# Optimization experiments

Hardware: AMD Instinct MI355X
Metric: run time of the kernel (lower is better)

## Reference

```python
import jax, jax.numpy as jnp
import numpy as np

B, F, H, E, O = 512, 512, 512, 8, 512  # batch, feature, hidden, experts, out_frame


def setup_inputs() -> dict:
    key = jax.random.key(0)
    ks = jax.random.split(key, 14)
    u = lambda k, shape, s: jax.random.uniform(k, shape, jnp.float32) * s
    return {
        "x": jax.random.normal(ks[0], (B, F), jnp.float32),
        # gating MLP params (torch Linear: y = x @ W.T + b)
        "gw0": u(ks[1], (H, F), 0.04) - 0.02,
        "gb0": jnp.zeros((H,), jnp.float32),
        "gw1": u(ks[2], (H, H), 0.04) - 0.02,
        "gb1": jnp.zeros((H,), jnp.float32),
        "gw2": u(ks[3], (E, H), 0.04) - 0.02,
        "gb2": jnp.zeros((E,), jnp.float32),
        # expert weight/bias banks
        "alpha0": u(ks[4], (E, H, F), 0.01),
        "beta0": jnp.zeros((E, H, 1), jnp.float32),
        "alpha1": u(ks[5], (E, H, H), 0.01),
        "beta1": jnp.zeros((E, H, 1), jnp.float32),
        "alpha2": u(ks[6], (E, O, H), 0.01),
        "beta2": jnp.zeros((E, O, 1), jnp.float32),
    }


def reference(x, gw0, gb0, gw1, gb1, gw2, gb2,
              alpha0, beta0, alpha1, beta1, alpha2, beta2):
    # gating network
    h = jax.nn.elu(x @ gw0.T + gb0)
    h = jax.nn.elu(h @ gw1.T + gb1)
    g = jax.nn.softmax(h @ gw2.T + gb2, axis=1)  # [B, E]

    # per-sample blended weights (sum over experts of gate-scaled expert mats)
    blend_w = lambda a: jnp.einsum('be,ehf->bhf', g, a)
    blend_b = lambda b: jnp.einsum('be,eh->bh', g, b[..., 0])

    # per-sample 3-layer MLP (bmm with vector rhs == batched matvec)
    H1 = jax.nn.elu(jnp.einsum('bhf,bf->bh', blend_w(alpha0), x) + blend_b(beta0))
    H2 = jax.nn.elu(jnp.einsum('bhf,bf->bh', blend_w(alpha1), H1) + blend_b(beta1))
    H3 = jnp.einsum('bof,bf->bo', blend_w(alpha2), H2) + blend_b(beta2)
    return H3
```

## Files before the change

### kernel.cpp

```cpp
#include <hip/hip_runtime.h>
#include <hip/hip_bf16.h>
#include <math.h>

enum { Bq = 512, Fq = 512, Hq = 512, Eq = 8, Oq = 512 };

typedef __attribute__((ext_vector_type(8))) short short8;
typedef __attribute__((ext_vector_type(4))) float floatx4;

static __device__ __forceinline__ unsigned short f2bf(float f) {
  unsigned u = __float_as_uint(f);
  u += 0x7fffu + ((u >> 16) & 1u);
  return (unsigned short)(u >> 16);
}
static __device__ __forceinline__ float bf2f(unsigned short h) {
  return __uint_as_float(((unsigned)h) << 16);
}
static __device__ __forceinline__ float elu1(float v) {
  return v > 0.f ? v : (__expf(v) - 1.f);
}

typedef __attribute__((address_space(1))) const unsigned int gu32;
typedef __attribute__((address_space(3))) unsigned int lu32;
static __device__ __forceinline__ void gld16(const unsigned short* g,
                                             unsigned short* l) {
  __builtin_amdgcn_global_load_lds((gu32*)g, (lu32*)l, 16, 0, 0);
}

__global__ __launch_bounds__(256) void cvt6_kernel(
    const float* __restrict__ b0, const float* __restrict__ b1,
    const float* __restrict__ b2, unsigned short* __restrict__ db0,
    unsigned short* __restrict__ db1, unsigned short* __restrict__ db2,
    const float* __restrict__ s0, const float* __restrict__ s1,
    const float* __restrict__ s2, unsigned short* __restrict__ ds0,
    unsigned short* __restrict__ ds1, unsigned short* __restrict__ ds2,
    int nb, int ns) {
  int i = blockIdx.x * 256 + threadIdx.x;
  const float4* s;
  unsigned short* d;
  int j;
  if (i < 3 * nb) {
    int seg = i / nb;
    j = i - seg * nb;
    s = (seg == 0) ? (const float4*)b0
      : (seg == 1) ? (const float4*)b1 : (const float4*)b2;
    d = (seg == 0) ? db0 : (seg == 1) ? db1 : db2;
  } else {
    int k = i - 3 * nb;
    if (k >= 3 * ns) return;
    int seg = k / ns;
    j = k - seg * ns;
    s = (seg == 0) ? (const float4*)s0
      : (seg == 1) ? (const float4*)s1 : (const float4*)s2;
    d = (seg == 0) ? ds0 : (seg == 1) ? ds1 : ds2;
  }
  float4 v = s[j];
  ushort4 o;
  o.x = f2bf(v.x); o.y = f2bf(v.y); o.z = f2bf(v.z); o.w = f2bf(v.w);
  *(ushort4*)(d + 4 * (size_t)j) = o;
}

template <int BM, int BN, int BK, int TM, int TN>
__global__ __launch_bounds__(256) void gemm_bt(
    const unsigned short* __restrict__ A, const unsigned short* __restrict__ W,
    const float* __restrict__ bias, unsigned short* __restrict__ Cb,
    int M, int N, int K) {
  __shared__ unsigned short As[BM * BK];
  __shared__ unsigned short Bs[BN * BK];
  const int tid = threadIdx.x;
  const int wave = tid >> 6, lane = tid & 63;
  const int wm = wave >> 1, wn = wave & 1;
  const int lr = lane & 15, lk = lane >> 4;
  const int m0 = blockIdx.y * BM, n0 = blockIdx.x * BN;
  constexpr int WMt = BM / 2, WNt = BN / 2;
  constexpr int CPR = BK / 8;
  constexpr int CHA = BM * CPR, CHB = BN * CPR;

  floatx4 acc[TM][TN];
#pragma unroll
  for (int i = 0; i < TM; i++)
#pragma unroll
    for (int j = 0; j < TN; j++) acc[i][j] = (floatx4){0.f, 0.f, 0.f, 0.f};

  for (int k0 = 0; k0 < K; k0 += BK) {
#pragma unroll
    for (int c = tid; c < CHA; c += 256) {
      int r = c / CPR, q = c % CPR;
      gld16(&A[(size_t)(m0 + r) * K + k0 + q * 8], &As[(c & ~63) * 8]);
    }
#pragma unroll
    for (int c = tid; c < CHB; c += 256) {
      int r = c / CPR, q = c % CPR;
      gld16(&W[(size_t)(n0 + r) * K + k0 + q * 8], &Bs[(c & ~63) * 8]);
    }
    __syncthreads();
#pragma unroll
    for (int kk = 0; kk < BK; kk += 32) {
      short8 af[TM], bw[TN];
#pragma unroll
      for (int i = 0; i < TM; i++)
        af[i] = *(const short8*)&As[(wm * WMt + i * 16 + lr) * BK + kk + lk * 8];
#pragma unroll
      for (int j = 0; j < TN; j++)
        bw[j] = *(const short8*)&Bs[(wn * WNt + j * 16 + lr) * BK + kk + lk * 8];
#pragma unroll
      for (int i = 0; i < TM; i++)
#pragma unroll
        for (int j = 0; j < TN; j++)
          acc[i][j] = __builtin_amdgcn_mfma_f32_16x16x32_bf16(
              af[i], bw[j], acc[i][j], 0, 0, 0);
    }
    __syncthreads();
  }

#pragma unroll
  for (int i = 0; i < TM; i++) {
#pragma unroll
    for (int j = 0; j < TN; j++) {
#pragma unroll
      for (int r = 0; r < 4; r++) {
        int m = m0 + wm * WMt + i * 16 + lk * 4 + r;
        int n = n0 + wn * WNt + j * 16 + lr;
        float v = acc[i][j][r] + bias[n];
        Cb[(size_t)m * N + n] = f2bf(elu1(v));
      }
    }
  }
}

template <int BM, int BN, int BK, int TM, int TN>
__global__ __launch_bounds__(256) void expert_gemm(
    const unsigned short* __restrict__ A,
    const unsigned short* __restrict__ Wb,
    const float* __restrict__ g,
    float* __restrict__ P) {
  __shared__ unsigned short As[BM * BK];
  __shared__ unsigned short Bs[BN * BK];
  const int tid = threadIdx.x;
  const int wave = tid >> 6, lane = tid & 63;
  const int wm = wave >> 1, wn = wave & 1;
  const int lr = lane & 15, lk = lane >> 4;
  const int m0 = blockIdx.y * BM, n0 = blockIdx.x * BN;
  const int e = blockIdx.z >> 1, ks = blockIdx.z & 1;
  const int kbeg = ks * 256, kend = kbeg + 256;
  const unsigned short* W = Wb + (size_t)e * Hq * 512 + (size_t)n0 * 512;
  constexpr int WMt = BM / 2, WNt = BN / 2;
  constexpr int CPR = BK / 8;
  constexpr int CHA = BM * CPR, CHB = BN * CPR;

  floatx4 acc[TM][TN];
#pragma unroll
  for (int i = 0; i < TM; i++)
#pragma unroll
    for (int j = 0; j < TN; j++) acc[i][j] = (floatx4){0.f, 0.f, 0.f, 0.f};

  for (int k0 = kbeg; k0 < kend; k0 += BK) {
#pragma unroll
    for (int c = tid; c < CHA; c += 256) {
      int r = c / CPR, q = c % CPR;
      gld16(&A[(size_t)(m0 + r) * 512 + k0 + q * 8], &As[(c & ~63) * 8]);
    }
#pragma unroll
    for (int c = tid; c < CHB; c += 256) {
      int r = c / CPR, q = c % CPR;
      gld16(&W[(size_t)r * 512 + k0 + q * 8], &Bs[(c & ~63) * 8]);
    }
    __syncthreads();
#pragma unroll
    for (int kk = 0; kk < BK; kk += 32) {
      short8 af[TM], bw[TN];
#pragma unroll
      for (int i = 0; i < TM; i++)
        af[i] = *(const short8*)&As[(wm * WMt + i * 16 + lr) * BK + kk + lk * 8];
#pragma unroll
      for (int j = 0; j < TN; j++)
        bw[j] = *(const short8*)&Bs[(wn * WNt + j * 16 + lr) * BK + kk + lk * 8];
#pragma unroll
      for (int i = 0; i < TM; i++)
#pragma unroll
        for (int j = 0; j < TN; j++)
          acc[i][j] = __builtin_amdgcn_mfma_f32_16x16x32_bf16(
              af[i], bw[j], acc[i][j], 0, 0, 0);
    }
    __syncthreads();
  }

  float* Po = P + (size_t)blockIdx.z * Bq * Hq;
#pragma unroll
  for (int i = 0; i < TM; i++) {
#pragma unroll
    for (int j = 0; j < TN; j++) {
#pragma unroll
      for (int r = 0; r < 4; r++) {
        int m = m0 + wm * WMt + i * 16 + lk * 4 + r;
        int n = n0 + wn * WNt + j * 16 + lr;
        Po[(size_t)m * Hq + n] = acc[i][j][r] * g[m * Eq + e];
      }
    }
  }
}

__global__ __launch_bounds__(64) void gate_kernel(
    const unsigned short* __restrict__ G1,
    const float* __restrict__ gw2,
    const float* __restrict__ gb2,
    float* __restrict__ g) {
  int b = blockIdx.x;
  int lane = threadIdx.x;
  float xv[8];
#pragma unroll
  for (int t = 0; t < 8; t++) xv[t] = bf2f(G1[(size_t)b * Hq + t * 64 + lane]);
  float le[Eq];
#pragma unroll
  for (int e = 0; e < Eq; e++) {
    float p = 0.f;
#pragma unroll
    for (int t = 0; t < 8; t++)
      p += xv[t] * gw2[(size_t)e * Hq + t * 64 + lane];
#pragma unroll
    for (int o = 32; o > 0; o >>= 1) p += __shfl_xor(p, o);
    le[e] = p + gb2[e];
  }
  float m = le[0];
#pragma unroll
  for (int e = 1; e < Eq; e++) m = fmaxf(m, le[e]);
  float s = 0.f;
#pragma unroll
  for (int e = 0; e < Eq; e++) {
    le[e] = __expf(le[e] - m);
    s += le[e];
  }
  float inv = 1.f / s;
  if (lane == 0) {
#pragma unroll
    for (int e = 0; e < Eq; e++) g[(size_t)b * Eq + e] = le[e] * inv;
  }
}

template <int ACT>
__global__ __launch_bounds__(256) void reduce_kernel(
    const float* __restrict__ P,
    const float* __restrict__ g,
    const float* __restrict__ beta,
    unsigned short* __restrict__ outb, float* __restrict__ outf) {
  int idx = blockIdx.x * 256 + threadIdx.x;
  int b = idx >> 7, h4 = (idx & 127) << 2;
  float4 s = {0.f, 0.f, 0.f, 0.f};
#pragma unroll
  for (int z = 0; z < 16; z++) {
    float4 v = *(const float4*)&P[((size_t)z * Bq + b) * Hq + h4];
    s.x += v.x; s.y += v.y; s.z += v.z; s.w += v.w;
  }
  const float* gb = g + (size_t)b * Eq;
#pragma unroll
  for (int e = 0; e < Eq; e++) {
    float ge = gb[e];
    float4 bv = *(const float4*)&beta[e * Hq + h4];
    s.x += ge * bv.x; s.y += ge * bv.y; s.z += ge * bv.z; s.w += ge * bv.w;
  }
  if (ACT) {
    ushort4 o;
    o.x = f2bf(elu1(s.x)); o.y = f2bf(elu1(s.y));
    o.z = f2bf(elu1(s.z)); o.w = f2bf(elu1(s.w));
    *(ushort4*)&outb[(size_t)idx * 4] = o;
  } else {
    *(float4*)&outf[(size_t)idx * 4] = s;
  }
}

extern "C" void kernel_launch(void* const* d_in, const int* in_sizes, int n_in,
                              void* d_out, int out_size, void* d_ws,
                              size_t ws_size, hipStream_t stream) {
  const float* x = (const float*)d_in[0];
  const float* gw0 = (const float*)d_in[1];
  const float* gb0 = (const float*)d_in[2];
  const float* gw1 = (const float*)d_in[3];
  const float* gb1 = (const float*)d_in[4];
  const float* gw2 = (const float*)d_in[5];
  const float* gb2 = (const float*)d_in[6];
  const float* alpha0 = (const float*)d_in[7];
  const float* beta0 = (const float*)d_in[8];
  const float* alpha1 = (const float*)d_in[9];
  const float* beta1 = (const float*)d_in[10];
  const float* alpha2 = (const float*)d_in[11];
  const float* beta2 = (const float*)d_in[12];
  float* out = (float*)d_out;

  char* ws = (char*)d_ws;
  auto alloc = [&](size_t bytes) {
    char* p = ws;
    ws += (bytes + 255) & ~(size_t)255;
    return p;
  };
  unsigned short* xb = (unsigned short*)alloc((size_t)Bq * Fq * 2);
  unsigned short* gw0b = (unsigned short*)alloc((size_t)Hq * Fq * 2);
  unsigned short* gw1b = (unsigned short*)alloc((size_t)Hq * Hq * 2);
  unsigned short* a0b = (unsigned short*)alloc((size_t)Eq * Hq * Fq * 2);
  unsigned short* a1b = (unsigned short*)alloc((size_t)Eq * Hq * Hq * 2);
  unsigned short* a2b = (unsigned short*)alloc((size_t)Eq * Oq * Hq * 2);
  unsigned short* G0b = (unsigned short*)alloc((size_t)Bq * Hq * 2);
  unsigned short* G1b = (unsigned short*)alloc((size_t)Bq * Hq * 2);
  unsigned short* H1b = (unsigned short*)alloc((size_t)Bq * Hq * 2);
  unsigned short* H2b = (unsigned short*)alloc((size_t)Bq * Hq * 2);
  float* gates = (float*)alloc((size_t)Bq * Eq * 4);
  float* P = (float*)alloc((size_t)16 * Bq * Hq * 4);

  {
    int nb = (Eq * Hq * Fq) / 4, ns = (Bq * Fq) / 4;
    int total = 3 * nb + 3 * ns;
    cvt6_kernel<<<(total + 255) / 256, 256, 0, stream>>>(
        alpha0, alpha1, alpha2, a0b, a1b, a2b, x, gw0, gw1, xb, gw0b, gw1b,
        nb, ns);
  }

  dim3 gg(Hq / 64, Bq / 32);
  gemm_bt<32, 64, 64, 1, 2><<<gg, 256, 0, stream>>>(xb, gw0b, gb0, G0b,
                                                    Bq, Hq, Fq);
  gemm_bt<32, 64, 64, 1, 2><<<gg, 256, 0, stream>>>(G0b, gw1b, gb1, G1b,
                                                    Bq, Hq, Hq);

  gate_kernel<<<Bq, 64, 0, stream>>>(G1b, gw2, gb2, gates);

  dim3 ge(Hq / 128, Bq / 64, Eq * 2);
  dim3 gr((Bq * Hq / 4) / 256);
  expert_gemm<64, 128, 64, 2, 4><<<ge, 256, 0, stream>>>(xb, a0b, gates, P);
  reduce_kernel<1><<<gr, 256, 0, stream>>>(P, gates, beta0, H1b, nullptr);
  expert_gemm<64, 128, 64, 2, 4><<<ge, 256, 0, stream>>>(H1b, a1b, gates, P);
  reduce_kernel<1><<<gr, 256, 0, stream>>>(P, gates, beta1, H2b, nullptr);
  expert_gemm<64, 128, 64, 2, 4><<<ge, 256, 0, stream>>>(H2b, a2b, gates, P);
  reduce_kernel<0><<<gr, 256, 0, stream>>>(P, gates, beta2, nullptr, out);
}
```

Before: 164.2 us.

## Load full K-slab into swizzled LDS in single pass for gating and expert GEMMs

Both GEMM kernels now load their whole K range (512 for gating, 256 per split for experts) into LDS at once, with an XOR swizzle to avoid bank conflicts, which removes the per-BK loop and its barriers. Gating tiles shrink to 32x32 with four independent k-partial accumulators, giving 256 blocks. Expert tiles shrink to 64x64 and the grid is reorganized to 64x8x2, raising block count to spread work across CUs. The cost is a much larger LDS footprint per block (64 KB gating), which lowers occupancy, and no overlap of loads with compute.

```diff
diff --git a/kernel.cpp b/kernel.cpp
--- a/kernel.cpp
+++ b/kernel.cpp
@@ -24,6 +24,10 @@
 static __device__ __forceinline__ void gld16(const unsigned short* g,
                                              unsigned short* l) {
   __builtin_amdgcn_global_load_lds((gu32*)g, (lu32*)l, 16, 0, 0);
+}
+
+static __device__ __forceinline__ int swz(int q, int r) {
+  return (q & ~7) | ((q ^ r) & 7);
 }
 
 __global__ __launch_bounds__(256) void cvt6_kernel(
@@ -59,141 +63,125 @@
   *(ushort4*)(d + 4 * (size_t)j) = o;
 }
 
-template <int BM, int BN, int BK, int TM, int TN>
-__global__ __launch_bounds__(256) void gemm_bt(
+__global__ __launch_bounds__(256) void gating_gemm(
     const unsigned short* __restrict__ A, const unsigned short* __restrict__ W,
-    const float* __restrict__ bias, unsigned short* __restrict__ Cb,
-    int M, int N, int K) {
-  __shared__ unsigned short As[BM * BK];
-  __shared__ unsigned short Bs[BN * BK];
+    const float* __restrict__ bias, unsigned short* __restrict__ C) {
+  __shared__ unsigned short As[32 * 512];
+  __shared__ unsigned short Ws[32 * 512];
   const int tid = threadIdx.x;
   const int wave = tid >> 6, lane = tid & 63;
   const int wm = wave >> 1, wn = wave & 1;
   const int lr = lane & 15, lk = lane >> 4;
-  const int m0 = blockIdx.y * BM, n0 = blockIdx.x * BN;
-  constexpr int WMt = BM / 2, WNt = BN / 2;
-  constexpr int CPR = BK / 8;
-  constexpr int CHA = BM * CPR, CHB = BN * CPR;
-
-  floatx4 acc[TM][TN];
-#pragma unroll
-  for (int i = 0; i < TM; i++)
-#pragma unroll
-    for (int j = 0; j < TN; j++) acc[i][j] = (floatx4){0.f, 0.f, 0.f, 0.f};
-
-  for (int k0 = 0; k0 < K; k0 += BK) {
-#pragma unroll
-    for (int c = tid; c < CHA; c += 256) {
-      int r = c / CPR, q = c % CPR;
-      gld16(&A[(size_t)(m0 + r) * K + k0 + q * 8], &As[(c & ~63) * 8]);
+  const int m0 = blockIdx.y * 32, n0 = blockIdx.x * 32;
+#pragma unroll
+  for (int i = 0; i < 8; i++) {
+    int c = tid + i * 256;
+    int r = c >> 6, ql = c & 63;
+    int qg = swz(ql, r);
+    gld16(&A[(size_t)(m0 + r) * 512 + qg * 8], &As[(c & ~63) * 8]);
+  }
+#pragma unroll
+  for (int i = 0; i < 8; i++) {
+    int c = tid + i * 256;
+    int r = c >> 6, ql = c & 63;
+    int qg = swz(ql, r);
+    gld16(&W[(size_t)(n0 + r) * 512 + qg * 8], &Ws[(c & ~63) * 8]);
+  }
+  __syncthreads();
+  const int rA = wm * 16 + lr, rB = wn * 16 + lr;
+  floatx4 ac[4];
+#pragma unroll
+  for (int j = 0; j < 4; j++) ac[j] = (floatx4){0.f, 0.f, 0.f, 0.f};
+#pragma unroll
+  for (int t = 0; t < 4; t++) {
+#pragma unroll
+    for (int j = 0; j < 4; j++) {
+      int q = ((j * 128 + t * 32) >> 3) + lk;
+      short8 av = *(const short8*)&As[rA * 512 + swz(q, rA) * 8];
+      short8 bv = *(const short8*)&Ws[rB * 512 + swz(q, rB) * 8];
+      ac[j] = __builtin_amdgcn_mfma_f32_16x16x32_bf16(av, bv, ac[j], 0, 0, 0);
     }
-#pragma unroll
-    for (int c = tid; c < CHB; c += 256) {
-      int r = c / CPR, q = c % CPR;
-      gld16(&W[(size_t)(n0 + r) * K + k0 + q * 8], &Bs[(c & ~63) * 8]);
-    }
-    __syncthreads();
-#pragma unroll
-    for (int kk = 0; kk < BK; kk += 32) {
-      short8 af[TM], bw[TN];
-#pragma unroll
-      for (int i = 0; i < TM; i++)
-        af[i] = *(const short8*)&As[(wm * WMt + i * 16 + lr) * BK + kk + lk * 8];
-#pragma unroll
-      for (int j = 0; j < TN; j++)
-        bw[j] = *(const short8*)&Bs[(wn * WNt + j * 16 + lr) * BK + kk + lk * 8];
-#pragma unroll
-      for (int i = 0; i < TM; i++)
-#pragma unroll
-        for (int j = 0; j < TN; j++)
-          acc[i][j] = __builtin_amdgcn_mfma_f32_16x16x32_bf16(
-              af[i], bw[j], acc[i][j], 0, 0, 0);
-    }
-    __syncthreads();
-  }
-
-#pragma unroll
-  for (int i = 0; i < TM; i++) {
-#pragma unroll
-    for (int j = 0; j < TN; j++) {
-#pragma unroll
-      for (int r = 0; r < 4; r++) {
-        int m = m0 + wm * WMt + i * 16 + lk * 4 + r;
-        int n = n0 + wn * WNt + j * 16 + lr;
-        float v = acc[i][j][r] + bias[n];
-        Cb[(size_t)m * N + n] = f2bf(elu1(v));
-      }
-    }
-  }
-}
-
-template <int BM, int BN, int BK, int TM, int TN>
+  }
+  floatx4 acc = (ac[0] + ac[1]) + (ac[2] + ac[3]);
+  int n = n0 + wn * 16 + lr;
+  float bn = bias[n];
+#pragma unroll
+  for (int r = 0; r < 4; r++) {
+    int m = m0 + wm * 16 + lk * 4 + r;
+    C[(size_t)m * 512 + n] = f2bf(elu1(acc[r] + bn));
+  }
+}
+
 __global__ __launch_bounds__(256) void expert_gemm(
     const unsigned short* __restrict__ A,
     const unsigned short* __restrict__ Wb,
     const float* __restrict__ g,
     float* __restrict__ P) {
-  __shared__ unsigned short As[BM * BK];
-  __shared__ unsigned short Bs[BN * BK];
+  __shared__ unsigned short As[64 * 256];
+  __shared__ unsigned short Ws[64 * 256];
   const int tid = threadIdx.x;
   const int wave = tid >> 6, lane = tid & 63;
   const int wm = wave >> 1, wn = wave & 1;
   const int lr = lane & 15, lk = lane >> 4;
-  const int m0 = blockIdx.y * BM, n0 = blockIdx.x * BN;
-  const int e = blockIdx.z >> 1, ks = blockIdx.z & 1;
-  const int kbeg = ks * 256, kend = kbeg + 256;
-  const unsigned short* W = Wb + (size_t)e * Hq * 512 + (size_t)n0 * 512;
-  constexpr int WMt = BM / 2, WNt = BN / 2;
-  constexpr int CPR = BK / 8;
-  constexpr int CHA = BM * CPR, CHB = BN * CPR;
-
-  floatx4 acc[TM][TN];
-#pragma unroll
-  for (int i = 0; i < TM; i++)
-#pragma unroll
-    for (int j = 0; j < TN; j++) acc[i][j] = (floatx4){0.f, 0.f, 0.f, 0.f};
-
-  for (int k0 = kbeg; k0 < kend; k0 += BK) {
-#pragma unroll
-    for (int c = tid; c < CHA; c += 256) {
-      int r = c / CPR, q = c % CPR;
-      gld16(&A[(size_t)(m0 + r) * 512 + k0 + q * 8], &As[(c & ~63) * 8]);
+  const int nt = blockIdx.x;
+  const int m0 = blockIdx.y * 64;
+  const int ks = blockIdx.z;
+  const int e = nt >> 3;
+  const int n0g = nt * 64;
+  const int n0l = (nt & 7) * 64;
+  const int kbeg = ks * 256;
+#pragma unroll
+  for (int i = 0; i < 8; i++) {
+    int c = tid + i * 256;
+    int r = c >> 5, ql = c & 31;
+    int qg = swz(ql, r);
+    gld16(&A[(size_t)(m0 + r) * 512 + kbeg + qg * 8], &As[(c & ~63) * 8]);
+  }
+#pragma unroll
+  for (int i = 0; i < 8; i++) {
+    int c = tid + i * 256;
+    int r = c >> 5, ql = c & 31;
+    int qg = swz(ql, r);
+    gld16(&Wb[(size_t)(n0g + r) * 512 + kbeg + qg * 8], &Ws[(c & ~63) * 8]);
+  }
+  __syncthreads();
+  floatx4 acc[2][2];
+#pragma unroll
+  for (int i = 0; i < 2; i++)
+#pragma unroll
+    for (int j = 0; j < 2; j++) acc[i][j] = (floatx4){0.f, 0.f, 0.f, 0.f};
+  const int rA0 = wm * 32 + lr, rB0 = wn * 32 + lr;
+#pragma unroll
+  for (int kk = 0; kk < 256; kk += 32) {
+    int q = (kk >> 3) + lk;
+    short8 af[2], bf[2];
+#pragma unroll
+    for (int i = 0; i < 2; i++) {
+      int r = rA0 + i * 16;
+      af[i] = *(const short8*)&As[r * 256 + swz(q, r) * 8];
     }
 #pragma unroll
-    for (int c = tid; c < CHB; c += 256) {
-      int r = c / CPR, q = c % CPR;
-      gld16(&W[(size_t)r * 512 + k0 + q * 8], &Bs[(c & ~63) * 8]);
+    for (int j = 0; j < 2; j++) {
+      int r = rB0 + j * 16;
+      bf[j] = *(const short8*)&Ws[r * 256 + swz(q, r) * 8];
     }
-    __syncthreads();
-#pragma unroll
-    for (int kk = 0; kk < BK; kk += 32) {
-      short8 af[TM], bw[TN];
-#pragma unroll
-      for (int i = 0; i < TM; i++)
-        af[i] = *(const short8*)&As[(wm * WMt + i * 16 + lr) * BK + kk + lk * 8];
-#pragma unroll
-      for (int j = 0; j < TN; j++)
-        bw[j] = *(const short8*)&Bs[(wn * WNt + j * 16 + lr) * BK + kk + lk * 8];
-#pragma unroll
-      for (int i = 0; i < TM; i++)
-#pragma unroll
-        for (int j = 0; j < TN; j++)
-          acc[i][j] = __builtin_amdgcn_mfma_f32_16x16x32_bf16(
-              af[i], bw[j], acc[i][j], 0, 0, 0);
-    }
-    __syncthreads();
-  }
-
-  float* Po = P + (size_t)blockIdx.z * Bq * Hq;
-#pragma unroll
-  for (int i = 0; i < TM; i++) {
-#pragma unroll
-    for (int j = 0; j < TN; j++) {
+#pragma unroll
+    for (int i = 0; i < 2; i++)
+#pragma unroll
+      for (int j = 0; j < 2; j++)
+        acc[i][j] = __builtin_amdgcn_mfma_f32_16x16x32_bf16(af[i], bf[j],
+                                                            acc[i][j], 0, 0, 0);
+  }
+  float* Po = P + (size_t)(ks * 8 + e) * Bq * Hq;
+#pragma unroll
+  for (int i = 0; i < 2; i++) {
+#pragma unroll
+    for (int j = 0; j < 2; j++) {
 #pragma unroll
       for (int r = 0; r < 4; r++) {
-        int m = m0 + wm * WMt + i * 16 + lk * 4 + r;
-        int n = n0 + wn * WNt + j * 16 + lr;
-        Po[(size_t)m * Hq + n] = acc[i][j][r] * g[m * Eq + e];
+        int m = m0 + wm * 32 + i * 16 + lk * 4 + r;
+        int n = n0l + wn * 32 + j * 16 + lr;
+        Po[(size_t)m * 512 + n] = acc[i][j][r] * g[m * Eq + e];
       }
     }
   }
@@ -312,20 +300,18 @@
         nb, ns);
   }
 
-  dim3 gg(Hq / 64, Bq / 32);
-  gemm_bt<32, 64, 64, 1, 2><<<gg, 256, 0, stream>>>(xb, gw0b, gb0, G0b,
-                                                    Bq, Hq, Fq);
-  gemm_bt<32, 64, 64, 1, 2><<<gg, 256, 0, stream>>>(G0b, gw1b, gb1, G1b,
-                                                    Bq, Hq, Hq);
+  dim3 gg(16, 16);
+  gating_gemm<<<gg, 256, 0, stream>>>(xb, gw0b, gb0, G0b);
+  gating_gemm<<<gg, 256, 0, stream>>>(G0b, gw1b, gb1, G1b);
 
   gate_kernel<<<Bq, 64, 0, stream>>>(G1b, gw2, gb2, gates);
 
-  dim3 ge(Hq / 128, Bq / 64, Eq * 2);
+  dim3 ge(64, 8, 2);
   dim3 gr((Bq * Hq / 4) / 256);
-  expert_gemm<64, 128, 64, 2, 4><<<ge, 256, 0, stream>>>(xb, a0b, gates, P);
+  expert_gemm<<<ge, 256, 0, stream>>>(xb, a0b, gates, P);
   reduce_kernel<1><<<gr, 256, 0, stream>>>(P, gates, beta0, H1b, nullptr);
-  expert_gemm<64, 128, 64, 2, 4><<<ge, 256, 0, stream>>>(H1b, a1b, gates, P);
+  expert_gemm<<<ge, 256, 0, stream>>>(H1b, a1b, gates, P);
   reduce_kernel<1><<<gr, 256, 0, stream>>>(P, gates, beta1, H2b, nullptr);
-  expert_gemm<64, 128, 64, 2, 4><<<ge, 256, 0, stream>>>(H2b, a2b, gates, P);
+  expert_gemm<<<ge, 256, 0, stream>>>(H2b, a2b, gates, P);
   reduce_kernel<0><<<gr, 256, 0, stream>>>(P, gates, beta2, nullptr, out);
 }
```

After: 149.5 us. 9.0% less time.
